# Kernel tuning notes

Hardware: AMD Instinct MI355X
Metric: run time of the kernel (lower is better)

The kernel has to match this reference:

```python
import jax, jax.numpy as jnp
import numpy as np

VOCAB, NUM_LABELS, EMB, H = 50000, 5, 512, 1024
B, S = 32, 256


def setup_inputs() -> dict:
    key = jax.random.key(0)
    ks = jax.random.split(key, 7)
    tokens = jax.random.randint(ks[0], (B, S), 0, VOCAB)
    scale_e = 0.05
    emb = jax.random.normal(ks[1], (VOCAB, EMB), dtype=jnp.float32) * scale_e
    # Keras LSTM kernels: input kernel [EMB,4H], recurrent kernel [H,4H], bias [4H]
    W = jax.random.normal(ks[2], (EMB, 4 * H), dtype=jnp.float32) / np.sqrt(EMB)
    U = jax.random.normal(ks[3], (H, 4 * H), dtype=jnp.float32) / np.sqrt(H)
    # unit_forget_bias=True: forget-gate bias block initialized to 1
    b = jnp.concatenate([
        jnp.zeros((H,), jnp.float32),
        jnp.ones((H,), jnp.float32),
        jnp.zeros((2 * H,), jnp.float32),
    ])
    Wd = jax.random.normal(ks[4], (H, NUM_LABELS), dtype=jnp.float32) / np.sqrt(H)
    bd = jnp.zeros((NUM_LABELS,), jnp.float32)
    return {"tokens": tokens, "emb": emb, "W": W, "U": U, "b": b, "Wd": Wd, "bd": bd}


def _lstm_last_h(x, W, U, b):
    # x: [B,S,EMB] -> last hidden state [B,H]
    xt = jnp.swapaxes(x, 0, 1)  # [S,B,EMB]
    # precompute input projections for all steps: [S,B,4H]
    xz = jnp.einsum('sbe,eg->sbg', xt, W) + b
    h0 = jnp.zeros((x.shape[0], H), x.dtype)
    c0 = jnp.zeros((x.shape[0], H), x.dtype)

    def step(carry, xz_t):
        h, c = carry
        z = xz_t + h @ U  # [B,4H]
        i, f, g, o = jnp.split(z, 4, axis=-1)  # Keras gate order i,f,c,o
        i = jax.nn.sigmoid(i)
        f = jax.nn.sigmoid(f)
        g = jnp.tanh(g)
        o = jax.nn.sigmoid(o)
        c = f * c + i * g
        h = o * jnp.tanh(c)
        return (h, c), None

    (h_last, _), _ = jax.lax.scan(step, (h0, c0), xz)
    return h_last


def reference(tokens, emb, W, U, b, Wd, bd):
    x = emb[tokens]  # [B,S,EMB] embedding lookup
    h = _lstm_last_h(x, W, U, b)  # [B,H]
    logits = h @ Wd + bd  # [B,NUM_LABELS]
    return logits
```

## Files before the change

kernel.cpp:

```cpp
#include <hip/hip_runtime.h>
#include <hip/hip_fp16.h>

#define B_   32
#define S_   256
#define EMB_ 512
#define H_   1024
#define G4_  4096
#define NL_  5
#define NBLK 128

typedef _Float16 f16x8 __attribute__((ext_vector_type(8)));
typedef float f32x4 __attribute__((ext_vector_type(4)));
typedef unsigned long long ull;

__device__ inline ull ldq(const ull* p) {
  return __hip_atomic_load(p, __ATOMIC_RELAXED, __HIP_MEMORY_SCOPE_AGENT);
}
__device__ inline unsigned ldw(const unsigned* p) {
  return __hip_atomic_load(p, __ATOMIC_RELAXED, __HIP_MEMORY_SCOPE_AGENT);
}
__device__ inline void stw(unsigned* p, unsigned v) {
  __hip_atomic_store(p, v, __ATOMIC_RELAXED, __HIP_MEMORY_SCOPE_AGENT);
}
__device__ inline float sigm(float x) {
  return __builtin_amdgcn_rcpf(1.f + __expf(-x));
}
__device__ inline float ftanh(float x) {
  float e = __expf(2.f * x);
  return (e - 1.f) * __builtin_amdgcn_rcpf(e + 1.f);
}

__global__ __launch_bounds__(256) void k_transposeK(const float* __restrict__ src,
                                                    float* __restrict__ dst, int K) {
  __shared__ float tile[32][33];
  int c0 = blockIdx.x * 32, k0 = blockIdx.y * 32;
  int tx = threadIdx.x & 31, ty = threadIdx.x >> 5;
#pragma unroll
  for (int i = 0; i < 4; ++i)
    tile[ty + 8 * i][tx] = src[(size_t)(k0 + ty + 8 * i) * G4_ + c0 + tx];
  __syncthreads();
#pragma unroll
  for (int i = 0; i < 4; ++i)
    dst[(size_t)(c0 + ty + 8 * i) * K + k0 + tx] = tile[tx][ty + 8 * i];
}

__global__ __launch_bounds__(256) void k_prepU16(const float* __restrict__ Ut,
                                                 f16x8* __restrict__ Ubf) {
  int gid = blockIdx.x * 256 + threadIdx.x;
  int l = gid & 63;
  int bxws = gid >> 6;
  int n = l & 15, kgrp = l >> 4;
  int s = bxws & 7, bw = bxws >> 3;
  int w = bw & 3, bx = bw >> 2;
  int g = n & 3, ju = n >> 2;
  int gcol = g * 1024 + bx * 4 + ju;
  int kbase = w * 256 + s * 32 + kgrp * 8;
  const float4* f = (const float4*)(Ut + (size_t)gcol * H_ + kbase);
  float4 f0 = f[0], f1 = f[1];
  float v[8] = {f0.x, f0.y, f0.z, f0.w, f1.x, f1.y, f1.z, f1.w};
  f16x8 vh, vl;
#pragma unroll
  for (int j = 0; j < 8; ++j) {
    _Float16 hi = (_Float16)v[j];
    vh[j] = hi;
    vl[j] = (_Float16)((v[j] - (float)hi) * 1024.f);
  }
  Ubf[(size_t)bxws * 128 + l] = vh;
  Ubf[(size_t)bxws * 128 + 64 + l] = vl;
}

__global__ __launch_bounds__(256) void k_prepW16(const float* __restrict__ Wt,
                                                 unsigned short* __restrict__ Wf16) {
  int gid = blockIdx.x * 256 + threadIdx.x;
  int l = gid & 63, fi = gid >> 6;
  int kc = fi & 15, ug = fi >> 4;
  int n16 = l & 15, kgrp = l >> 4;
  int gcol = (n16 & 3) * 1024 + ug * 4 + (n16 >> 2);
  const float4* f = (const float4*)(Wt + (size_t)gcol * 512 + kc * 32 + kgrp * 8);
  float4 f0 = f[0], f1 = f[1];
  float v[8] = {f0.x, f0.y, f0.z, f0.w, f1.x, f1.y, f1.z, f1.w};
  union { unsigned short u[8]; uint4 q; } o;
#pragma unroll
  for (int j = 0; j < 8; ++j) o.u[j] = __half_as_ushort(__float2half_rn(v[j]));
  *(uint4*)(Wf16 + ((size_t)fi * 64 + l) * 8) = o.q;
}

__global__ __launch_bounds__(256) void k_prepX(const int* __restrict__ tokens,
                                               const float* __restrict__ emb,
                                               unsigned short* __restrict__ Xf16) {
  int gid = blockIdx.x * 256 + threadIdx.x;
  int seg = gid & 63, row = gid >> 6;
  int s = row >> 5, b = row & 31;
  int tok = tokens[b * 256 + s];
  const float4* f = (const float4*)(emb + (size_t)tok * EMB_ + seg * 8);
  float4 f0 = f[0], f1 = f[1];
  float v[8] = {f0.x, f0.y, f0.z, f0.w, f1.x, f1.y, f1.z, f1.w};
  union { unsigned short u[8]; uint4 q; } o;
#pragma unroll
  for (int j = 0; j < 8; ++j) o.u[j] = __half_as_ushort(__float2half_rn(v[j]));
  *(uint4*)(Xf16 + (size_t)row * 512 + seg * 8) = o.q;
}

__global__ __launch_bounds__(512, 2) void k_steps12(
    const f16x8* __restrict__ Ubf,
    const unsigned short* __restrict__ Wf16,
    const unsigned short* __restrict__ Xf16,
    const float* __restrict__ bias,
    unsigned* __restrict__ T0, unsigned* __restrict__ T1,
    unsigned* __restrict__ flg) {
  __shared__ f16x8 UL[4096];
  __shared__ float red[2][8192];
  __shared__ float zg[2][1056];
  __shared__ float bias_s[32];

  const int tid = threadIdx.x;
  const int bx = blockIdx.x;
  const int l = tid & 63, w = tid >> 6;

#pragma unroll
  for (int i = 0; i < 8; ++i) {
    int flat = i * 512 + tid;
    int ll = flat & 63, s8 = (flat >> 6) & 7, ks = (flat >> 9) & 3;
    int cg = flat >> 11;
    size_t fi = (size_t)((bx * 2 + cg) * 4 + ks) * 8 + s8;
    UL[flat] = Ubf[fi * 128 + ll];
  }
  if (tid < 32) {
    int cg = tid >> 4, n16 = tid & 15;
    bias_s[tid] = bias[(n16 & 3) * 1024 + (bx * 2 + cg) * 4 + (n16 >> 2)];
  }

  const int e = tid & 255, m = tid >> 8;
  const int n16r = (e >> 2) & 15;
  const int zb = m * 16 + (e >> 6) * 4 + (e & 3);

  const int gb = tid & 31, gu = tid >> 5;
  const int widx = (((gb >> 4) * 128 + bx) * 16 + (gb & 15)) * 4 + (gu >> 1);
  const int zrd = gb * 33 + (gu >> 2) * 16 + (gu & 3) * 4;
  float creg = 0.f;

  const int ks_w = w >> 1;
  const int xrow0 = (l & 15) * 512 + (l >> 4) * 8;
  const unsigned* myflg = flg + (size_t)((w * 16 + (l >> 2)) * 4 + (l & 3)) * 16;

  __syncthreads();

  for (int t = 0; t < S_; ++t) {
    const int par = t & 1;
    const ull* R64 = (const ull*)(par ? T0 : T1);
    unsigned* WrT = par ? T1 : T0;

    f16x8 ulo[4][2];
#pragma unroll
    for (int s = 0; s < 4; ++s)
#pragma unroll
      for (int cg = 0; cg < 2; ++cg)
        ulo[s][cg] = Ubf[((size_t)((bx * 2 + cg) * 4 + ks_w) * 8 +
                          (w & 1) * 4 + s) * 128 + 64 + l];

    f32x4 acc[2][2], accL[2][2];
#pragma unroll
    for (int cg = 0; cg < 2; ++cg)
#pragma unroll
      for (int m2 = 0; m2 < 2; ++m2) {
        acc[cg][m2] = (f32x4){0.f, 0.f, 0.f, 0.f};
        accL[cg][m2] = (f32x4){0.f, 0.f, 0.f, 0.f};
      }
    {
      const unsigned short* Xt = Xf16 + (size_t)t * 16384;
#pragma unroll
      for (int c2 = 0; c2 < 2; ++c2) {
        int kc = w * 2 + c2;
        f16x8 xa0 = *(const f16x8*)(Xt + xrow0 + kc * 32);
        f16x8 xa1 = *(const f16x8*)(Xt + 8192 + xrow0 + kc * 32);
        f16x8 wb0 = *(const f16x8*)(Wf16 + ((size_t)((bx * 2 + 0) * 16 + kc) * 64 + l) * 8);
        f16x8 wb1 = *(const f16x8*)(Wf16 + ((size_t)((bx * 2 + 1) * 16 + kc) * 64 + l) * 8);
        acc[0][0] = __builtin_amdgcn_mfma_f32_16x16x32_f16(xa0, wb0, acc[0][0], 0, 0, 0);
        acc[0][1] = __builtin_amdgcn_mfma_f32_16x16x32_f16(xa1, wb0, acc[0][1], 0, 0, 0);
        acc[1][0] = __builtin_amdgcn_mfma_f32_16x16x32_f16(xa0, wb1, acc[1][0], 0, 0, 0);
        acc[1][1] = __builtin_amdgcn_mfma_f32_16x16x32_f16(xa1, wb1, acc[1][1], 0, 0, 0);
      }
    }

    if (t > 0) {
      const unsigned tg = (unsigned)t;
      while (true) {
        unsigned v = ldw(myflg);
        if (__all((int)(v >= tg))) break;
        __builtin_amdgcn_s_sleep(1);
      }
      union F { ull q[2]; f16x8 v; };
      F A[2][4];
#pragma unroll
      for (int m2 = 0; m2 < 2; ++m2)
#pragma unroll
        for (int s = 0; s < 4; ++s) {
          int kidx = w * 16 + s * 4 + (l >> 4);
          int b64 = ((m2 * 128 + kidx) * 16 + (l & 15)) * 2;
          A[m2][s].q[0] = ldq(R64 + b64);
          A[m2][s].q[1] = ldq(R64 + b64 + 1);
        }
#pragma unroll
      for (int s = 0; s < 4; ++s) {
        int s8 = (w & 1) * 4 + s;
#pragma unroll
        for (int cg = 0; cg < 2; ++cg) {
          f16x8 uhf = UL[cg * 2048 + ks_w * 512 + s8 * 64 + l];
          acc[cg][0]  = __builtin_amdgcn_mfma_f32_16x16x32_f16(A[0][s].v, uhf, acc[cg][0], 0, 0, 0);
          acc[cg][1]  = __builtin_amdgcn_mfma_f32_16x16x32_f16(A[1][s].v, uhf, acc[cg][1], 0, 0, 0);
          accL[cg][0] = __builtin_amdgcn_mfma_f32_16x16x32_f16(A[0][s].v, ulo[s][cg], accL[cg][0], 0, 0, 0);
          accL[cg][1] = __builtin_amdgcn_mfma_f32_16x16x32_f16(A[1][s].v, ulo[s][cg], accL[cg][1], 0, 0, 0);
        }
      }
    }

#pragma unroll
    for (int cg = 0; cg < 2; ++cg)
#pragma unroll
      for (int m2 = 0; m2 < 2; ++m2)
        acc[cg][m2] += accL[cg][m2] * 9.765625e-4f;

#pragma unroll
    for (int cg = 0; cg < 2; ++cg)
#pragma unroll
      for (int m2 = 0; m2 < 2; ++m2)
        *(f32x4*)(&red[par][(w * 4 + m2 * 2 + cg) * 256 + l * 4]) = acc[cg][m2];
    __syncthreads();

    {
      float z0 = bias_s[n16r], z1 = bias_s[16 + n16r];
#pragma unroll
      for (int ww = 0; ww < 8; ++ww) {
        z0 += red[par][(ww * 4 + m * 2 + 0) * 256 + e];
        z1 += red[par][(ww * 4 + m * 2 + 1) * 256 + e];
      }
      zg[par][zb * 33 + n16r] = z0;
      zg[par][zb * 33 + 16 + n16r] = z1;
    }
    __syncthreads();

    if (tid < 256) {
      float zi = zg[par][zrd + 0];
      float zf = zg[par][zrd + 1];
      float zc = zg[par][zrd + 2];
      float zo = zg[par][zrd + 3];
      float ig = sigm(zi);
      float fg = sigm(zf);
      float gg = ftanh(zc);
      float og = sigm(zo);
      creg = fg * creg + ig * gg;
      float hv = og * ftanh(creg);
      unsigned pk = (unsigned)__half_as_ushort(__float2half_rn(hv));
      unsigned other = (unsigned)__shfl_xor((int)pk, 32, 64);
      if ((gu & 1) == 0)
        stw(WrT + widx, (pk & 0xffffu) | (other << 16));
      asm volatile("s_waitcnt vmcnt(0)" ::: "memory");
      if ((tid & 63) == 0)
        stw(flg + (size_t)(bx * 4 + (tid >> 6)) * 16, (unsigned)(t + 1));
    }
  }
}

__global__ __launch_bounds__(256) void k_head6(const unsigned* __restrict__ T,
                                               const float* __restrict__ Wd,
                                               const float* __restrict__ bd,
                                               float* __restrict__ out) {
  __shared__ float red[32 * 9];
  int lbl = blockIdx.x;
  int tid = threadIdx.x;
  int b = tid >> 3, ks = tid & 7;
  float acc = 0.f;
  for (int k = ks * 128; k < ks * 128 + 128; ++k) {
    int idx = (((b >> 4) * 128 + (k >> 3)) * 16 + (b & 15)) * 4 + ((k & 7) >> 1);
    unsigned wv = T[idx];
    unsigned short h16 = (unsigned short)((k & 1) ? (wv >> 16) : (wv & 0xffffu));
    acc += __half2float(__ushort_as_half(h16)) * Wd[k * NL_ + lbl];
  }
  red[b * 9 + ks] = acc;
  __syncthreads();
  if (tid < 32) {
    float s = bd[lbl];
#pragma unroll
    for (int i = 0; i < 8; ++i) s += red[tid * 9 + i];
    out[tid * NL_ + lbl] = s;
  }
}

extern "C" void kernel_launch(void* const* d_in, const int* in_sizes, int n_in,
                              void* d_out, int out_size, void* d_ws, size_t ws_size,
                              hipStream_t stream) {
  const int* tokens  = (const int*)d_in[0];
  const float* emb   = (const float*)d_in[1];
  const float* W     = (const float*)d_in[2];
  const float* U     = (const float*)d_in[3];
  const float* bias  = (const float*)d_in[4];
  const float* Wd    = (const float*)d_in[5];
  const float* bd    = (const float*)d_in[6];
  float* out = (float*)d_out;

  char* ws = (char*)d_ws;
  unsigned short* Xf16 = (unsigned short*)ws;
  unsigned short* Wf16 = (unsigned short*)(ws + 8388608);
  float* Ut          = (float*)(ws + 16777216);
  float* Wt          = (float*)(ws + 33554432);
  f16x8* Ubf         = (f16x8*)(ws + 41943040);
  unsigned* T0       = (unsigned*)(ws + 58720256);
  unsigned* T1       = (unsigned*)(ws + 58785792);
  unsigned* flg      = (unsigned*)(ws + 58851328);

  hipMemsetAsync(flg, 0, 32768, stream);
  k_transposeK<<<dim3(128, 32), 256, 0, stream>>>(U, Ut, 1024);
  k_prepU16<<<2048, 256, 0, stream>>>(Ut, Ubf);
  k_transposeK<<<dim3(128, 16), 256, 0, stream>>>(W, Wt, 512);
  k_prepW16<<<1024, 256, 0, stream>>>(Wt, Wf16);
  k_prepX<<<2048, 256, 0, stream>>>(tokens, emb, Xf16);

  k_steps12<<<NBLK, 512, 0, stream>>>(Ubf, Wf16, Xf16, bias, T0, T1, flg);

  k_head6<<<NL_, 256, 0, stream>>>(T1, Wd, bd, out);
}
```

Measured before the change: 1.039 ms.

## Pack step flags densely and poll with 64-bit loads; defer input MFMAs past wait

Per-wave completion flags are now packed contiguously instead of each sitting on its own 64-byte stride. Each lane polls four flags with two 64-bit atomic loads, so the spin loop issues fewer, denser loads. The input-projection loads are issued before the wait, but their MFMAs now run after the h loads are posted, so X/W fetch latency overlaps the spin. Packing the flags puts several writers on one cache line, which may add contention between producers and pollers.

```diff
diff --git a/kernel.cpp b/kernel.cpp
--- a/kernel.cpp
+++ b/kernel.cpp
@@ -101,7 +101,7 @@
   *(uint4*)(Xf16 + (size_t)row * 512 + seg * 8) = o.q;
 }
 
-__global__ __launch_bounds__(512, 2) void k_steps12(
+__global__ __launch_bounds__(512, 2) void k_steps13(
     const f16x8* __restrict__ Ubf,
     const unsigned short* __restrict__ Wf16,
     const unsigned short* __restrict__ Xf16,
@@ -141,7 +141,7 @@
 
   const int ks_w = w >> 1;
   const int xrow0 = (l & 15) * 512 + (l >> 4) * 8;
-  const unsigned* myflg = flg + (size_t)((w * 16 + (l >> 2)) * 4 + (l & 3)) * 16;
+  const ull* myflg = (const ull*)(flg + (size_t)(w * 16 + (l & 15)) * 4);
 
   __syncthreads();
 
@@ -158,6 +158,19 @@
         ulo[s][cg] = Ubf[((size_t)((bx * 2 + cg) * 4 + ks_w) * 8 +
                           (w & 1) * 4 + s) * 128 + 64 + l];
 
+    f16x8 xa[2][2], wb[2][2];
+    {
+      const unsigned short* Xt = Xf16 + (size_t)t * 16384;
+#pragma unroll
+      for (int c2 = 0; c2 < 2; ++c2) {
+        int kc = w * 2 + c2;
+        xa[c2][0] = *(const f16x8*)(Xt + xrow0 + kc * 32);
+        xa[c2][1] = *(const f16x8*)(Xt + 8192 + xrow0 + kc * 32);
+        wb[c2][0] = *(const f16x8*)(Wf16 + ((size_t)((bx * 2 + 0) * 16 + kc) * 64 + l) * 8);
+        wb[c2][1] = *(const f16x8*)(Wf16 + ((size_t)((bx * 2 + 1) * 16 + kc) * 64 + l) * 8);
+      }
+    }
+
     f32x4 acc[2][2], accL[2][2];
 #pragma unroll
     for (int cg = 0; cg < 2; ++cg)
@@ -166,31 +179,18 @@
         acc[cg][m2] = (f32x4){0.f, 0.f, 0.f, 0.f};
         accL[cg][m2] = (f32x4){0.f, 0.f, 0.f, 0.f};
       }
-    {
-      const unsigned short* Xt = Xf16 + (size_t)t * 16384;
-#pragma unroll
-      for (int c2 = 0; c2 < 2; ++c2) {
-        int kc = w * 2 + c2;
-        f16x8 xa0 = *(const f16x8*)(Xt + xrow0 + kc * 32);
-        f16x8 xa1 = *(const f16x8*)(Xt + 8192 + xrow0 + kc * 32);
-        f16x8 wb0 = *(const f16x8*)(Wf16 + ((size_t)((bx * 2 + 0) * 16 + kc) * 64 + l) * 8);
-        f16x8 wb1 = *(const f16x8*)(Wf16 + ((size_t)((bx * 2 + 1) * 16 + kc) * 64 + l) * 8);
-        acc[0][0] = __builtin_amdgcn_mfma_f32_16x16x32_f16(xa0, wb0, acc[0][0], 0, 0, 0);
-        acc[0][1] = __builtin_amdgcn_mfma_f32_16x16x32_f16(xa1, wb0, acc[0][1], 0, 0, 0);
-        acc[1][0] = __builtin_amdgcn_mfma_f32_16x16x32_f16(xa0, wb1, acc[1][0], 0, 0, 0);
-        acc[1][1] = __builtin_amdgcn_mfma_f32_16x16x32_f16(xa1, wb1, acc[1][1], 0, 0, 0);
-      }
-    }
-
+
+    union F { ull q[2]; f16x8 v; };
+    F A[2][4];
     if (t > 0) {
       const unsigned tg = (unsigned)t;
       while (true) {
-        unsigned v = ldw(myflg);
-        if (__all((int)(v >= tg))) break;
+        ull q0 = ldq(myflg), q1 = ldq(myflg + 1);
+        bool ok = ((unsigned)q0 >= tg) && ((unsigned)(q0 >> 32) >= tg) &&
+                  ((unsigned)q1 >= tg) && ((unsigned)(q1 >> 32) >= tg);
+        if (__all((int)ok)) break;
         __builtin_amdgcn_s_sleep(1);
       }
-      union F { ull q[2]; f16x8 v; };
-      F A[2][4];
 #pragma unroll
       for (int m2 = 0; m2 < 2; ++m2)
 #pragma unroll
@@ -200,6 +200,17 @@
           A[m2][s].q[0] = ldq(R64 + b64);
           A[m2][s].q[1] = ldq(R64 + b64 + 1);
         }
+    }
+
+#pragma unroll
+    for (int c2 = 0; c2 < 2; ++c2) {
+      acc[0][0] = __builtin_amdgcn_mfma_f32_16x16x32_f16(xa[c2][0], wb[c2][0], acc[0][0], 0, 0, 0);
+      acc[0][1] = __builtin_amdgcn_mfma_f32_16x16x32_f16(xa[c2][1], wb[c2][0], acc[0][1], 0, 0, 0);
+      acc[1][0] = __builtin_amdgcn_mfma_f32_16x16x32_f16(xa[c2][0], wb[c2][1], acc[1][0], 0, 0, 0);
+      acc[1][1] = __builtin_amdgcn_mfma_f32_16x16x32_f16(xa[c2][1], wb[c2][1], acc[1][1], 0, 0, 0);
+    }
+
+    if (t > 0) {
 #pragma unroll
       for (int s = 0; s < 4; ++s) {
         int s8 = (w & 1) * 4 + s;
@@ -256,7 +267,7 @@
         stw(WrT + widx, (pk & 0xffffu) | (other << 16));
       asm volatile("s_waitcnt vmcnt(0)" ::: "memory");
       if ((tid & 63) == 0)
-        stw(flg + (size_t)(bx * 4 + (tid >> 6)) * 16, (unsigned)(t + 1));
+        stw(flg + (size_t)(bx * 4 + (tid >> 6)), (unsigned)(t + 1));
     }
   }
 }
@@ -308,14 +319,14 @@
   unsigned* T1       = (unsigned*)(ws + 58785792);
   unsigned* flg      = (unsigned*)(ws + 58851328);
 
-  hipMemsetAsync(flg, 0, 32768, stream);
+  hipMemsetAsync(flg, 0, 4096, stream);
   k_transposeK<<<dim3(128, 32), 256, 0, stream>>>(U, Ut, 1024);
   k_prepU16<<<2048, 256, 0, stream>>>(Ut, Ubf);
   k_transposeK<<<dim3(128, 16), 256, 0, stream>>>(W, Wt, 512);
   k_prepW16<<<1024, 256, 0, stream>>>(Wt, Wf16);
   k_prepX<<<2048, 256, 0, stream>>>(tokens, emb, Xf16);
 
-  k_steps12<<<NBLK, 512, 0, stream>>>(Ubf, Wf16, Xf16, bias, T0, T1, flg);
+  k_steps13<<<NBLK, 512, 0, stream>>>(Ubf, Wf16, Xf16, bias, T0, T1, flg);
 
   k_head6<<<NL_, 256, 0, stream>>>(T1, Wd, bd, out);
 }
```

Result: slower. 1.570 ms (+51.1%).
